# Kernel optimization log

Measured on AMD Instinct MI355X. Metric: run time of the kernel, lower is better.

Reference implementation:

```python
import jax, jax.numpy as jnp
import numpy as np

B, S, HID = 2, 1024, 2048
HQ, HKV, HD = 32, 8, 64
ROPE_BASE = 10000.0

def _rope_tables(seq_len, head_dim):
    inv_freq = 1.0 / (ROPE_BASE ** (np.arange(0, head_dim, 2, dtype=np.float32) / head_dim))
    t = np.arange(seq_len, dtype=np.float32)
    freqs = np.outer(t, inv_freq)                      # [S, d/2]
    emb = np.concatenate([freqs, freqs], axis=-1)      # [S, d]
    return jnp.asarray(np.cos(emb)), jnp.asarray(np.sin(emb))

def setup_inputs() -> dict:
    key = jax.random.key(0)
    ks = jax.random.split(key, 5)
    cos, sin = _rope_tables(S, HD)
    return {
        'hidden_states': jax.random.normal(ks[0], (B, S, HID), jnp.float32),
        'cos': cos, 'sin': sin,
        'Wq': jax.random.normal(ks[1], (HID, HID), jnp.float32) * (HID ** -0.5),
        'Wk': jax.random.normal(ks[2], (HID, HKV * HD), jnp.float32) * (HID ** -0.5),
        'Wv': jax.random.normal(ks[3], (HID, HKV * HD), jnp.float32) * (HID ** -0.5),
        'Wo': jax.random.normal(ks[4], (HID, HID), jnp.float32) * (HID ** -0.5),
    }

def _rotate_half(x):
    d = x.shape[-1]
    return jnp.concatenate([-x[..., d // 2:], x[..., :d // 2]], axis=-1)

def reference(hidden_states, cos, sin, Wq, Wk, Wv, Wo):
    b, s, _ = hidden_states.shape
    q = (hidden_states @ Wq).reshape(b, s, HQ, HD)    # [b,s,Hq,d]
    k = (hidden_states @ Wk).reshape(b, s, HKV, HD)   # [b,s,Hkv,d]
    v = (hidden_states @ Wv).reshape(b, s, HKV, HD)
    # RoPE: cos/sin [s,d] broadcast as [s,1,d] over head dim
    c = cos[:, None, :]
    sn = sin[:, None, :]
    q = q * c + _rotate_half(q) * sn
    k = k * c + _rotate_half(k) * sn
    # GQA: expand kv heads to query heads (repeat_kv)
    n_rep = HQ // HKV
    k = jnp.repeat(k, n_rep, axis=2)                  # [b,s,Hq,d]
    v = jnp.repeat(v, n_rep, axis=2)
    scale = HD ** -0.5
    scores = jnp.einsum('bqhd,bkhd->bhqk', q, k) * scale  # [b,Hq,s,s]
    causal = jnp.tril(jnp.ones((s, s), bool))
    scores = jnp.where(causal, scores, jnp.float32(-1e30))
    probs = jax.nn.softmax(scores.astype(jnp.float32), axis=-1).astype(q.dtype)
    out = jnp.einsum('bhqk,bkhd->bqhd', probs, v).reshape(b, s, HID)
    return out @ Wo
```

## Files before the change

kernel.cpp:

```cpp
#include <hip/hip_runtime.h>
#include <math.h>

#define B_   2
#define S_   1024
#define HID_ 2048
#define HQ_  32
#define HKV_ 8
#define HD_  64
#define NQKV 3072

#define PCHUNK 2097152

using short8  = __attribute__((ext_vector_type(8))) short;
using floatx4 = __attribute__((ext_vector_type(4))) float;

__device__ __forceinline__ unsigned short f2bf(float x) {
    unsigned int u = __builtin_bit_cast(unsigned int, x);
    u += 0x7FFFu + ((u >> 16) & 1u);
    return (unsigned short)(u >> 16);
}
__device__ __forceinline__ float bf2f(unsigned short u) {
    return __builtin_bit_cast(float, (unsigned int)u << 16);
}

__device__ __forceinline__ void gl_lds16(const unsigned short* g, unsigned short* l) {
    __builtin_amdgcn_global_load_lds(
        (const __attribute__((address_space(1))) void*)g,
        (__attribute__((address_space(3))) void*)l, 16, 0, 0);
}

__global__ __launch_bounds__(256) void gemm_qkv(const unsigned short* __restrict__ A,
                                                const unsigned short* __restrict__ Bt,
                                                unsigned short* __restrict__ Qp,
                                                unsigned short* __restrict__ KVp) {
    __shared__ __align__(16) unsigned short As[128 * 32];
    __shared__ __align__(16) unsigned short Bs[128 * 32];

    int bid = blockIdx.x;
    int m0, n0, z, Nw, nc0;
    unsigned short* C;
    if (bid < 512) {
        n0 = (bid & 15) * 128; m0 = ((bid >> 4) & 15) * 128; z = bid >> 8;
        C = Qp + (size_t)z * 2048 * 2048; Nw = 2048; nc0 = n0;
    } else {
        bid -= 512;
        n0 = 2048 + (bid & 7) * 128; m0 = ((bid >> 3) & 15) * 128; z = bid >> 7;
        C = KVp + (size_t)z * 2048 * 1024; Nw = 1024; nc0 = n0 - 2048;
    }
    const int kbase = z * 1024;

    const int tid  = threadIdx.x;
    const int w    = tid >> 6;
    const int lane = tid & 63;
    const int col  = lane & 15;
    const int quad = lane >> 4;
    const int wm = (w >> 1) * 64;
    const int wn = (w & 1) * 64;

    const int srow = lane >> 2;
    const int skof = (lane & 3) * 8;
    const unsigned short* Ag = A  + (size_t)(m0 + srow) * HID_ + skof;
    const unsigned short* Bg = Bt + (size_t)(n0 + srow) * HID_ + skof;
    const int rb = w * 16;

    floatx4 acc[4][4] = {};

    for (int k0 = kbase; k0 < kbase + 1024; k0 += 32) {
        gl_lds16(Ag + (size_t)(rb     ) * HID_ + k0, &As[(rb     ) * 32]);
        gl_lds16(Ag + (size_t)(rb + 64) * HID_ + k0, &As[(rb + 64) * 32]);
        gl_lds16(Bg + (size_t)(rb     ) * HID_ + k0, &Bs[(rb     ) * 32]);
        gl_lds16(Bg + (size_t)(rb + 64) * HID_ + k0, &Bs[(rb + 64) * 32]);
        __syncthreads();

        short8 af[4], bfr[4];
#pragma unroll
        for (int i = 0; i < 4; ++i)
            af[i] = *(const short8*)&As[(wm + i * 16 + col) * 32 + quad * 8];
#pragma unroll
        for (int j = 0; j < 4; ++j)
            bfr[j] = *(const short8*)&Bs[(wn + j * 16 + col) * 32 + quad * 8];
#pragma unroll
        for (int i = 0; i < 4; ++i)
#pragma unroll
            for (int j = 0; j < 4; ++j)
                acc[i][j] = __builtin_amdgcn_mfma_f32_16x16x32_bf16(
                    af[i], bfr[j], acc[i][j], 0, 0, 0);
        __syncthreads();
    }

#pragma unroll
    for (int i = 0; i < 4; ++i)
#pragma unroll
        for (int j = 0; j < 4; ++j)
#pragma unroll
            for (int r = 0; r < 4; ++r)
                C[(size_t)(m0 + wm + i * 16 + quad * 4 + r) * Nw
                  + (nc0 + wn + j * 16 + col)] = f2bf(acc[i][j][r]);
}

__global__ __launch_bounds__(256) void gemm_wo(const unsigned short* __restrict__ A,
                                               const unsigned short* __restrict__ Bt,
                                               float* __restrict__ Cf,
                                               unsigned short* __restrict__ Cp1) {
    __shared__ __align__(16) unsigned short As[128 * 32];
    __shared__ __align__(16) unsigned short Bs[128 * 32];

    const int m0 = blockIdx.y * 128;
    const int n0 = blockIdx.x * 128;
    const int z  = blockIdx.z;
    const int kbase = z * 1024;

    const int tid  = threadIdx.x;
    const int w    = tid >> 6;
    const int lane = tid & 63;
    const int col  = lane & 15;
    const int quad = lane >> 4;
    const int wm = (w >> 1) * 64;
    const int wn = (w & 1) * 64;

    const int srow = lane >> 2;
    const int skof = (lane & 3) * 8;
    const unsigned short* Ag = A  + (size_t)(m0 + srow) * HID_ + skof;
    const unsigned short* Bg = Bt + (size_t)(n0 + srow) * HID_ + skof;
    const int rb = w * 16;

    floatx4 acc[4][4] = {};

    for (int k0 = kbase; k0 < kbase + 1024; k0 += 32) {
        gl_lds16(Ag + (size_t)(rb     ) * HID_ + k0, &As[(rb     ) * 32]);
        gl_lds16(Ag + (size_t)(rb + 64) * HID_ + k0, &As[(rb + 64) * 32]);
        gl_lds16(Bg + (size_t)(rb     ) * HID_ + k0, &Bs[(rb     ) * 32]);
        gl_lds16(Bg + (size_t)(rb + 64) * HID_ + k0, &Bs[(rb + 64) * 32]);
        __syncthreads();

        short8 af[4], bfr[4];
#pragma unroll
        for (int i = 0; i < 4; ++i)
            af[i] = *(const short8*)&As[(wm + i * 16 + col) * 32 + quad * 8];
#pragma unroll
        for (int j = 0; j < 4; ++j)
            bfr[j] = *(const short8*)&Bs[(wn + j * 16 + col) * 32 + quad * 8];
#pragma unroll
        for (int i = 0; i < 4; ++i)
#pragma unroll
            for (int j = 0; j < 4; ++j)
                acc[i][j] = __builtin_amdgcn_mfma_f32_16x16x32_bf16(
                    af[i], bfr[j], acc[i][j], 0, 0, 0);
        __syncthreads();
    }

#pragma unroll
    for (int i = 0; i < 4; ++i)
#pragma unroll
        for (int j = 0; j < 4; ++j)
#pragma unroll
            for (int r = 0; r < 4; ++r) {
                size_t off = (size_t)(m0 + wm + i * 16 + quad * 4 + r) * HID_
                           + (n0 + wn + j * 16 + col);
                if (z == 0) Cf[off] = acc[i][j][r];
                else        Cp1[off] = f2bf(acc[i][j][r]);
            }
}

__global__ __launch_bounds__(256) void reduce_wo(float* __restrict__ out,
                                                 const unsigned short* __restrict__ p1) {
    int i4 = (blockIdx.x * 256 + threadIdx.x) * 4;
    float4 o = *(float4*)&out[i4];
    ushort4 p = *(const ushort4*)&p1[i4];
    o.x += bf2f(p.x); o.y += bf2f(p.y); o.z += bf2f(p.z); o.w += bf2f(p.w);
    *(float4*)&out[i4] = o;
}

__global__ __launch_bounds__(256) void convert_x(const float* __restrict__ in,
                                                 unsigned short* __restrict__ out) {
    int tid = blockIdx.x * 256 + threadIdx.x;
    float4 v = *(const float4*)&in[(size_t)tid * 4];
    ushort4 o = {f2bf(v.x), f2bf(v.y), f2bf(v.z), f2bf(v.w)};
    *(ushort4*)&out[(size_t)tid * 4] = o;
}

__global__ __launch_bounds__(256) void transpose_qkv(const float* __restrict__ Wq,
                                                     const float* __restrict__ Wk,
                                                     const float* __restrict__ Wv,
                                                     unsigned short* __restrict__ WcatT) {
    __shared__ float tile[32][33];
    int bid = blockIdx.x;
    const float* W;
    unsigned short* WT;
    int N, tn0, tk0;
    if (bid < 4096) {
        W = Wq; WT = WcatT; N = HID_;
        tn0 = (bid & 63) * 32; tk0 = (bid >> 6) * 32;
    } else if (bid < 5120) {
        bid -= 4096;
        W = Wk; WT = WcatT + (size_t)HID_ * HID_; N = 512;
        tn0 = (bid & 15) * 32; tk0 = (bid >> 4) * 32;
    } else {
        bid -= 5120;
        W = Wv; WT = WcatT + (size_t)(HID_ + 512) * HID_; N = 512;
        tn0 = (bid & 15) * 32; tk0 = (bid >> 4) * 32;
    }
    const int r  = threadIdx.x >> 3;
    const int c4 = (threadIdx.x & 7) * 4;
    float4 v = *(const float4*)&W[(size_t)(tk0 + r) * N + tn0 + c4];
    tile[r][c4 + 0] = v.x;
    tile[r][c4 + 1] = v.y;
    tile[r][c4 + 2] = v.z;
    tile[r][c4 + 3] = v.w;
    __syncthreads();
    ushort4 o = {f2bf(tile[c4 + 0][r]), f2bf(tile[c4 + 1][r]),
                 f2bf(tile[c4 + 2][r]), f2bf(tile[c4 + 3][r])};
    *(ushort4*)&WT[(size_t)(tn0 + r) * HID_ + tk0 + c4] = o;
}

__global__ __launch_bounds__(256) void transpose_wo(const float* __restrict__ Wo,
                                                    unsigned short* __restrict__ WoT) {
    __shared__ float tile[32][33];
    int bid = blockIdx.x;
    const int tn0 = (bid & 63) * 32;
    const int tk0 = (bid >> 6) * 32;
    const int r  = threadIdx.x >> 3;
    const int c4 = (threadIdx.x & 7) * 4;
    float4 v = *(const float4*)&Wo[(size_t)(tk0 + r) * HID_ + tn0 + c4];
    tile[r][c4 + 0] = v.x;
    tile[r][c4 + 1] = v.y;
    tile[r][c4 + 2] = v.z;
    tile[r][c4 + 3] = v.w;
    __syncthreads();
    ushort4 o = {f2bf(tile[c4 + 0][r]), f2bf(tile[c4 + 1][r]),
                 f2bf(tile[c4 + 2][r]), f2bf(tile[c4 + 3][r])};
    *(ushort4*)&WoT[(size_t)(tn0 + r) * HID_ + tk0 + c4] = o;
}

__global__ __launch_bounds__(256) void convert_qkv(const unsigned short* __restrict__ Qp,
                                                   const unsigned short* __restrict__ KVp,
                                                   const float* __restrict__ cosT,
                                                   const float* __restrict__ sinT,
                                                   unsigned short* __restrict__ Qbf,
                                                   unsigned short* __restrict__ Kbf,
                                                   unsigned short* __restrict__ Vt) {
    const size_t QSTR  = (size_t)2048 * 2048;
    const size_t KVSTR = (size_t)2048 * 1024;
    int tid = blockIdx.x * 256 + threadIdx.x;
    const int NQ = B_ * S_ * HQ_ * 32;
    const int NK = B_ * S_ * HKV_ * 32;
    if (tid < NQ) {
        int d = tid & 31;
        int h = (tid >> 5) & (HQ_ - 1);
        int s = (tid >> 10) & (S_ - 1);
        int b = tid >> 20;
        const unsigned short* row = Qp + (size_t)(b * S_ + s) * 2048 + h * HD_;
        float x0 = bf2f(row[d])      + bf2f(row[QSTR + d]);
        float x1 = bf2f(row[d + 32]) + bf2f(row[QSTR + d + 32]);
        float c0 = cosT[s * HD_ + d],      s0 = sinT[s * HD_ + d];
        float c1 = cosT[s * HD_ + d + 32], s1 = sinT[s * HD_ + d + 32];
        unsigned short* orow = Qbf + ((size_t)(b * HQ_ + h) * S_ + s) * HD_;
        orow[d]      = f2bf((x0 * c0 - x1 * s0) * 0.125f);
        orow[d + 32] = f2bf((x1 * c1 + x0 * s1) * 0.125f);
    } else if (tid < NQ + NK) {
        tid -= NQ;
        int d  = tid & 31;
        int kv = (tid >> 5) & (HKV_ - 1);
        int s  = (tid >> 8) & (S_ - 1);
        int b  = tid >> 18;
        const unsigned short* row = KVp + (size_t)(b * S_ + s) * 1024 + kv * HD_;
        float x0 = bf2f(row[d])      + bf2f(row[KVSTR + d]);
        float x1 = bf2f(row[d + 32]) + bf2f(row[KVSTR + d + 32]);
        float c0 = cosT[s * HD_ + d],      s0 = sinT[s * HD_ + d];
        float c1 = cosT[s * HD_ + d + 32], s1 = sinT[s * HD_ + d + 32];
        unsigned short* orow = Kbf + ((size_t)(b * HKV_ + kv) * S_ + s) * HD_;
        orow[d]      = f2bf(x0 * c0 - x1 * s0);
        orow[d + 32] = f2bf(x1 * c1 + x0 * s1);
    } else {
        tid -= NQ + NK;
        int s4 = tid & 255;
        int d  = (tid >> 8) & (HD_ - 1);
        int kv = (tid >> 14) & (HKV_ - 1);
        int b  = tid >> 17;
        int s  = s4 * 4;
        const unsigned short* base =
            KVp + ((size_t)(b * S_ + s)) * 1024 + 512 + kv * HD_ + d;
        ushort4 o;
#pragma unroll
        for (int j = 0; j < 4; ++j) {
            float v = bf2f(base[(size_t)j * 1024]) +
                      bf2f(base[KVSTR + (size_t)j * 1024]);
            ((unsigned short*)&o)[j] = f2bf(v);
        }
        *(ushort4*)&Vt[((size_t)(b * HKV_ + kv) * HD_ + d) * S_ + s] = o;
    }
}

__global__ __launch_bounds__(256) void attn_mfma(const unsigned short* __restrict__ Qbf,
                                                 const unsigned short* __restrict__ Kbf,
                                                 const unsigned short* __restrict__ Vt,
                                                 unsigned short* __restrict__ Ctx,
                                                 float* __restrict__ PO,
                                                 float* __restrict__ ML) {
    const int x  = blockIdx.x;
    const int kv = blockIdx.y;
    const int b  = blockIdx.z;

    int tq, chunk, it0, it1;
    if (x < 32) {
        tq = 16 + (x >> 1); chunk = x & 1;
        const int ns = (32 * tq + 95) >> 6;
        const int hh = ns >> 1;
        it0 = chunk ? hh : 0;
        it1 = chunk ? ns : hh;
    } else {
        tq = 47 - x; chunk = -1;
        it0 = 0;
        it1 = (32 * tq + 95) >> 6;
    }

    const int w    = threadIdx.x >> 6;
    const int lane = threadIdx.x & 63;
    const int col  = lane & 15;
    const int quad = lane >> 4;

    const int h   = kv * 4 + w;
    const int bh  = b * HQ_ + h;
    const int bkv = b * HKV_ + kv;
    const int qw  = 32 * tq;

    __shared__ __align__(16) unsigned short sK[2][64 * 64];
    __shared__ __align__(16) unsigned short sV[2][64 * 64];
    __shared__ __align__(16) unsigned short sP[4][16 * 64];
    unsigned short* myP = sP[w];

    short8 bq[2][2];
#pragma unroll
    for (int u = 0; u < 2; ++u) {
        const unsigned short* qrow = Qbf + ((size_t)bh * S_ + qw + 16 * u + col) * HD_;
        bq[u][0] = *(const short8*)&qrow[quad * 8];
        bq[u][1] = *(const short8*)&qrow[32 + quad * 8];
    }

    const unsigned short* Kbase = Kbf + (size_t)bkv * S_ * HD_;
    const unsigned short* Vbase = Vt  + (size_t)bkv * HD_ * S_;

    const int sr  = lane >> 3;
    const int ssl = (lane & 7) ^ sr;
    const int r0  = 16 * w;

    floatx4 acc[2][4] = {};
    float m_i[2] = {-1e30f, -1e30f};
    float l_i[2] = {0.f, 0.f};

    {
        const int kb = it0 * 64;
#pragma unroll
        for (int c = 0; c < 2; ++c) {
            const int row = r0 + 8 * c + sr;
            gl_lds16(Kbase + (size_t)(kb + row) * HD_ + ssl * 8, &sK[0][(r0 + 8 * c) * 64]);
            gl_lds16(Vbase + (size_t)row * S_ + kb + ssl * 8,    &sV[0][(r0 + 8 * c) * 64]);
        }
    }
    __syncthreads();

    int cur = 0;
    for (int it = it0; it < it1; ++it) {
        const int k0 = it * 64;

        if (it + 1 < it1) {
            const int kn = k0 + 64;
#pragma unroll
            for (int c = 0; c < 2; ++c) {
                const int row = r0 + 8 * c + sr;
                gl_lds16(Kbase + (size_t)(kn + row) * HD_ + ssl * 8,
                         &sK[cur ^ 1][(r0 + 8 * c) * 64]);
                gl_lds16(Vbase + (size_t)row * S_ + kn + ssl * 8,
                         &sV[cur ^ 1][(r0 + 8 * c) * 64]);
            }
        }

        floatx4 sc[2][4];
        __builtin_amdgcn_s_setprio(1);
#pragma unroll
        for (int tt = 0; tt < 4; ++tt) {
            const int krow = 16 * tt + col;
            const unsigned short* kr = &sK[cur][krow * 64];
            short8 ak0 = *(const short8*)&kr[((quad    ) ^ (krow & 7)) * 8];
            short8 ak1 = *(const short8*)&kr[((quad + 4) ^ (krow & 7)) * 8];
#pragma unroll
            for (int u = 0; u < 2; ++u) {
                floatx4 z = {0.f, 0.f, 0.f, 0.f};
                z = __builtin_amdgcn_mfma_f32_16x16x32_bf16(ak0, bq[u][0], z, 0, 0, 0);
                z = __builtin_amdgcn_mfma_f32_16x16x32_bf16(ak1, bq[u][1], z, 0, 0, 0);
                sc[u][tt] = z;
            }
        }
        __builtin_amdgcn_s_setprio(0);

        short8 pa[2][2];
#pragma unroll
        for (int u = 0; u < 2; ++u) {
            const int qbase = qw + 16 * u;
            const int myq   = qbase + col;
            if (k0 + 63 > qbase) {
#pragma unroll
                for (int tt = 0; tt < 4; ++tt)
#pragma unroll
                    for (int r = 0; r < 4; ++r)
                        if (k0 + 16 * tt + quad * 4 + r > myq) sc[u][tt][r] = -1e30f;
            }
            float vmax = sc[u][0][0];
#pragma unroll
            for (int tt = 0; tt < 4; ++tt)
#pragma unroll
                for (int r = 0; r < 4; ++r)
                    vmax = fmaxf(vmax, sc[u][tt][r]);
            vmax = fmaxf(vmax, __shfl_xor(vmax, 16, 64));
            vmax = fmaxf(vmax, __shfl_xor(vmax, 32, 64));

            if (!__all(vmax <= m_i[u] + 8.0f)) {
                const float mnew  = fmaxf(m_i[u], vmax);
                const float alpha = __expf(m_i[u] - mnew);
                m_i[u] = mnew;
                l_i[u] *= alpha;
#pragma unroll
                for (int nt = 0; nt < 4; ++nt)
#pragma unroll
                    for (int r = 0; r < 4; ++r)
                        acc[u][nt][r] *= alpha;
            }
            const float mu = m_i[u];

            float lsum = 0.f;
#pragma unroll
            for (int tt = 0; tt < 4; ++tt) {
                float p0 = __expf(sc[u][tt][0] - mu);
                float p1 = __expf(sc[u][tt][1] - mu);
                float p2 = __expf(sc[u][tt][2] - mu);
                float p3 = __expf(sc[u][tt][3] - mu);
                lsum += (p0 + p1) + (p2 + p3);
                ushort4 pk = {f2bf(p0), f2bf(p1), f2bf(p2), f2bf(p3)};
                *(ushort4*)&myP[col * 64
                                + ((((4 * tt + quad) >> 1) ^ (col & 7)) << 3)
                                + (quad & 1) * 4] = pk;
            }
            lsum += __shfl_xor(lsum, 16, 64);
            lsum += __shfl_xor(lsum, 32, 64);
            l_i[u] += lsum;

            pa[u][0] = *(const short8*)&myP[col * 64 + (((quad    ) ^ (col & 7)) << 3)];
            pa[u][1] = *(const short8*)&myP[col * 64 + (((4 + quad) ^ (col & 7)) << 3)];
        }

        __builtin_amdgcn_s_setprio(1);
#pragma unroll
        for (int nt = 0; nt < 4; ++nt) {
            const int vrow = 16 * nt + col;
            const unsigned short* vr = &sV[cur][vrow * 64];
            short8 vb0 = *(const short8*)&vr[((quad    ) ^ (vrow & 7)) * 8];
            short8 vb1 = *(const short8*)&vr[((quad + 4) ^ (vrow & 7)) * 8];
#pragma unroll
            for (int u = 0; u < 2; ++u) {
                acc[u][nt] = __builtin_amdgcn_mfma_f32_16x16x32_bf16(vb0, pa[u][0], acc[u][nt], 0, 0, 0);
                acc[u][nt] = __builtin_amdgcn_mfma_f32_16x16x32_bf16(vb1, pa[u][1], acc[u][nt], 0, 0, 0);
            }
        }
        __builtin_amdgcn_s_setprio(0);

        __syncthreads();
        cur ^= 1;
    }

    if (chunk < 0) {
#pragma unroll
        for (int u = 0; u < 2; ++u) {
            const float invl = 1.0f / l_i[u];
            unsigned short* crow =
                Ctx + (size_t)(b * S_ + qw + 16 * u + col) * HID_ + h * HD_;
#pragma unroll
            for (int nt = 0; nt < 4; ++nt) {
                ushort4 o = {f2bf(acc[u][nt][0] * invl), f2bf(acc[u][nt][1] * invl),
                             f2bf(acc[u][nt][2] * invl), f2bf(acc[u][nt][3] * invl)};
                *(ushort4*)&crow[nt * 16 + quad * 4] = o;
            }
        }
    } else {
        const int ts = tq - 16;
        const int base_row = (((b * 8 + kv) * 16 + ts) * 4 + w) * 32;
        float* POc = PO + (size_t)chunk * PCHUNK;
#pragma unroll
        for (int u = 0; u < 2; ++u) {
            float* prow = &POc[(size_t)(base_row + 16 * u + col) * 64];
#pragma unroll
            for (int nt = 0; nt < 4; ++nt)
                *(floatx4*)&prow[nt * 16 + quad * 4] = acc[u][nt];
            if (quad == 0) {
                const int rr = chunk * 32768 + base_row + 16 * u + col;
                ML[rr * 2 + 0] = m_i[u];
                ML[rr * 2 + 1] = l_i[u];
            }
        }
    }
}

__global__ __launch_bounds__(256) void merge_attn(const float* __restrict__ PO,
                                                  const float* __restrict__ ML,
                                                  unsigned short* __restrict__ Ctx) {
    const int tid = blockIdx.x * 256 + threadIdx.x;
    const int i4  = tid * 4;
    const int row = i4 >> 6;
    const int d0  = i4 & 63;

    const float m0 = ML[row * 2 + 0];
    const float l0 = ML[row * 2 + 1];
    const float m1 = ML[(32768 + row) * 2 + 0];
    const float l1 = ML[(32768 + row) * 2 + 1];
    const float mf = fmaxf(m0, m1);
    const float s0 = __expf(m0 - mf);
    const float s1 = __expf(m1 - mf);
    const float inv = 1.0f / (l0 * s0 + l1 * s1);

    float4 o0 = *(const float4*)&PO[(size_t)row * 64 + d0];
    float4 o1 = *(const float4*)&PO[(size_t)PCHUNK + (size_t)row * 64 + d0];

    const int q  = row & 31;
    const int hh = (row >> 5) & 3;
    const int ts = (row >> 7) & 15;
    const int kv = (row >> 11) & 7;
    const int b  = row >> 14;
    const int q_abs = 512 + ts * 32 + q;
    const int h_abs = kv * 4 + hh;

    ushort4 o;
    o.x = f2bf((o0.x * s0 + o1.x * s1) * inv);
    o.y = f2bf((o0.y * s0 + o1.y * s1) * inv);
    o.z = f2bf((o0.z * s0 + o1.z * s1) * inv);
    o.w = f2bf((o0.w * s0 + o1.w * s1) * inv);
    *(ushort4*)&Ctx[((size_t)(b * S_ + q_abs)) * HID_ + h_abs * HD_ + d0] = o;
}

extern "C" void kernel_launch(void* const* d_in, const int* in_sizes, int n_in,
                              void* d_out, int out_size, void* d_ws, size_t ws_size,
                              hipStream_t stream) {
    const float* X    = (const float*)d_in[0];
    const float* cosT = (const float*)d_in[1];
    const float* sinT = (const float*)d_in[2];
    const float* Wq   = (const float*)d_in[3];
    const float* Wk   = (const float*)d_in[4];
    const float* Wv   = (const float*)d_in[5];
    const float* Wo   = (const float*)d_in[6];

    const int M = B_ * S_;
    const size_t MB = 1024u * 1024u;

    char* ws = (char*)d_ws;
    unsigned short* Xbf   = (unsigned short*)(ws);
    unsigned short* Qbf   = (unsigned short*)(ws);
    unsigned short* WcatT = (unsigned short*)(ws + 8 * MB);
    unsigned short* Kbf   = (unsigned short*)(ws + 8 * MB);
    unsigned short* Vt    = (unsigned short*)(ws + 10 * MB);
    float*          MLb   = (float*)(ws + 12 * MB);
    unsigned short* WoT   = (unsigned short*)(ws + 12 * MB);
    unsigned short* KVp   = (unsigned short*)(ws + 20 * MB);
    unsigned short* Ctxbf = (unsigned short*)(ws + 20 * MB);
    unsigned short* Wop1  = (unsigned short*)(ws);
    unsigned short* Qp    = (unsigned short*)d_out;
    float*          PO    = (float*)d_out;
    float* out = (float*)d_out;

    convert_x<<<(M * HID_ / 4) / 256, 256, 0, stream>>>(X, Xbf);

    transpose_qkv<<<6144, 256, 0, stream>>>(Wq, Wk, Wv, WcatT);

    gemm_qkv<<<768, 256, 0, stream>>>(Xbf, WcatT, Qp, KVp);

    {
        int total = B_ * S_ * HQ_ * 32 + B_ * S_ * HKV_ * 32
                  + B_ * HKV_ * HD_ * (S_ / 4);
        convert_qkv<<<total / 256, 256, 0, stream>>>(Qp, KVp, cosT, sinT,
                                                     Qbf, Kbf, Vt);
    }

    attn_mfma<<<dim3(48, HKV_, B_), 256, 0, stream>>>(Qbf, Kbf, Vt, Ctxbf,
                                                      PO, MLb);

    merge_attn<<<2048, 256, 0, stream>>>(PO, MLb, Ctxbf);

    transpose_wo<<<4096, 256, 0, stream>>>(Wo, WoT);

    gemm_wo<<<dim3(16, 16, 2), 256, 0, stream>>>(Ctxbf, WoT, out, Wop1);

    reduce_wo<<<(M * HID_ / 4) / 256, 256, 0, stream>>>(out, Wop1);
}
```

Measured before the change: 246.6 us.

## Deepen GEMM K-tile with swizzled LDS, fuse prep kernels, vectorize RoPE conversion

```diff
diff --git a/kernel.cpp b/kernel.cpp
--- a/kernel.cpp
+++ b/kernel.cpp
@@ -33,8 +33,8 @@
                                                 const unsigned short* __restrict__ Bt,
                                                 unsigned short* __restrict__ Qp,
                                                 unsigned short* __restrict__ KVp) {
-    __shared__ __align__(16) unsigned short As[128 * 32];
-    __shared__ __align__(16) unsigned short Bs[128 * 32];
+    __shared__ __align__(16) unsigned short As[128 * 64];
+    __shared__ __align__(16) unsigned short Bs[128 * 64];
 
     int bid = blockIdx.x;
     int m0, n0, z, Nw, nc0;
@@ -57,34 +57,39 @@
     const int wm = (w >> 1) * 64;
     const int wn = (w & 1) * 64;
 
-    const int srow = lane >> 2;
-    const int skof = (lane & 3) * 8;
-    const unsigned short* Ag = A  + (size_t)(m0 + srow) * HID_ + skof;
-    const unsigned short* Bg = Bt + (size_t)(n0 + srow) * HID_ + skof;
-    const int rb = w * 16;
+    const int srow = lane >> 3;
+    const int scol = ((lane & 7) ^ srow) * 8;
+    const unsigned short* Ag = A  + (size_t)(m0 + w * 32 + srow) * HID_ + scol;
+    const unsigned short* Bg = Bt + (size_t)(n0 + w * 32 + srow) * HID_ + scol;
 
     floatx4 acc[4][4] = {};
 
-    for (int k0 = kbase; k0 < kbase + 1024; k0 += 32) {
-        gl_lds16(Ag + (size_t)(rb     ) * HID_ + k0, &As[(rb     ) * 32]);
-        gl_lds16(Ag + (size_t)(rb + 64) * HID_ + k0, &As[(rb + 64) * 32]);
-        gl_lds16(Bg + (size_t)(rb     ) * HID_ + k0, &Bs[(rb     ) * 32]);
-        gl_lds16(Bg + (size_t)(rb + 64) * HID_ + k0, &Bs[(rb + 64) * 32]);
+    for (int k0 = kbase; k0 < kbase + 1024; k0 += 64) {
+#pragma unroll
+        for (int c = 0; c < 4; ++c) {
+            gl_lds16(Ag + (size_t)(8 * c) * HID_ + k0, &As[(w * 32 + 8 * c) * 64]);
+            gl_lds16(Bg + (size_t)(8 * c) * HID_ + k0, &Bs[(w * 32 + 8 * c) * 64]);
+        }
         __syncthreads();
 
-        short8 af[4], bfr[4];
-#pragma unroll
-        for (int i = 0; i < 4; ++i)
-            af[i] = *(const short8*)&As[(wm + i * 16 + col) * 32 + quad * 8];
-#pragma unroll
-        for (int j = 0; j < 4; ++j)
-            bfr[j] = *(const short8*)&Bs[(wn + j * 16 + col) * 32 + quad * 8];
-#pragma unroll
-        for (int i = 0; i < 4; ++i)
+#pragma unroll
+        for (int hh = 0; hh < 2; ++hh) {
+            short8 af[4], bfr[4];
+#pragma unroll
+            for (int i = 0; i < 4; ++i)
+                af[i] = *(const short8*)&As[(wm + i * 16 + col) * 64
+                                            + (((hh * 4 + quad) ^ (col & 7)) << 3)];
 #pragma unroll
             for (int j = 0; j < 4; ++j)
-                acc[i][j] = __builtin_amdgcn_mfma_f32_16x16x32_bf16(
-                    af[i], bfr[j], acc[i][j], 0, 0, 0);
+                bfr[j] = *(const short8*)&Bs[(wn + j * 16 + col) * 64
+                                             + (((hh * 4 + quad) ^ (col & 7)) << 3)];
+#pragma unroll
+            for (int i = 0; i < 4; ++i)
+#pragma unroll
+                for (int j = 0; j < 4; ++j)
+                    acc[i][j] = __builtin_amdgcn_mfma_f32_16x16x32_bf16(
+                        af[i], bfr[j], acc[i][j], 0, 0, 0);
+        }
         __syncthreads();
     }
 
@@ -102,8 +107,8 @@
                                                const unsigned short* __restrict__ Bt,
                                                float* __restrict__ Cf,
                                                unsigned short* __restrict__ Cp1) {
-    __shared__ __align__(16) unsigned short As[128 * 32];
-    __shared__ __align__(16) unsigned short Bs[128 * 32];
+    __shared__ __align__(16) unsigned short As[128 * 64];
+    __shared__ __align__(16) unsigned short Bs[128 * 64];
 
     const int m0 = blockIdx.y * 128;
     const int n0 = blockIdx.x * 128;
@@ -118,34 +123,39 @@
     const int wm = (w >> 1) * 64;
     const int wn = (w & 1) * 64;
 
-    const int srow = lane >> 2;
-    const int skof = (lane & 3) * 8;
-    const unsigned short* Ag = A  + (size_t)(m0 + srow) * HID_ + skof;
-    const unsigned short* Bg = Bt + (size_t)(n0 + srow) * HID_ + skof;
-    const int rb = w * 16;
+    const int srow = lane >> 3;
+    const int scol = ((lane & 7) ^ srow) * 8;
+    const unsigned short* Ag = A  + (size_t)(m0 + w * 32 + srow) * HID_ + scol;
+    const unsigned short* Bg = Bt + (size_t)(n0 + w * 32 + srow) * HID_ + scol;
 
     floatx4 acc[4][4] = {};
 
-    for (int k0 = kbase; k0 < kbase + 1024; k0 += 32) {
-        gl_lds16(Ag + (size_t)(rb     ) * HID_ + k0, &As[(rb     ) * 32]);
-        gl_lds16(Ag + (size_t)(rb + 64) * HID_ + k0, &As[(rb + 64) * 32]);
-        gl_lds16(Bg + (size_t)(rb     ) * HID_ + k0, &Bs[(rb     ) * 32]);
-        gl_lds16(Bg + (size_t)(rb + 64) * HID_ + k0, &Bs[(rb + 64) * 32]);
+    for (int k0 = kbase; k0 < kbase + 1024; k0 += 64) {
+#pragma unroll
+        for (int c = 0; c < 4; ++c) {
+            gl_lds16(Ag + (size_t)(8 * c) * HID_ + k0, &As[(w * 32 + 8 * c) * 64]);
+            gl_lds16(Bg + (size_t)(8 * c) * HID_ + k0, &Bs[(w * 32 + 8 * c) * 64]);
+        }
         __syncthreads();
 
-        short8 af[4], bfr[4];
-#pragma unroll
-        for (int i = 0; i < 4; ++i)
-            af[i] = *(const short8*)&As[(wm + i * 16 + col) * 32 + quad * 8];
-#pragma unroll
-        for (int j = 0; j < 4; ++j)
-            bfr[j] = *(const short8*)&Bs[(wn + j * 16 + col) * 32 + quad * 8];
-#pragma unroll
-        for (int i = 0; i < 4; ++i)
+#pragma unroll
+        for (int hh = 0; hh < 2; ++hh) {
+            short8 af[4], bfr[4];
+#pragma unroll
+            for (int i = 0; i < 4; ++i)
+                af[i] = *(const short8*)&As[(wm + i * 16 + col) * 64
+                                            + (((hh * 4 + quad) ^ (col & 7)) << 3)];
 #pragma unroll
             for (int j = 0; j < 4; ++j)
-                acc[i][j] = __builtin_amdgcn_mfma_f32_16x16x32_bf16(
-                    af[i], bfr[j], acc[i][j], 0, 0, 0);
+                bfr[j] = *(const short8*)&Bs[(wn + j * 16 + col) * 64
+                                             + (((hh * 4 + quad) ^ (col & 7)) << 3)];
+#pragma unroll
+            for (int i = 0; i < 4; ++i)
+#pragma unroll
+                for (int j = 0; j < 4; ++j)
+                    acc[i][j] = __builtin_amdgcn_mfma_f32_16x16x32_bf16(
+                        af[i], bfr[j], acc[i][j], 0, 0, 0);
+        }
         __syncthreads();
     }
 
@@ -171,34 +181,44 @@
     *(float4*)&out[i4] = o;
 }
 
-__global__ __launch_bounds__(256) void convert_x(const float* __restrict__ in,
-                                                 unsigned short* __restrict__ out) {
-    int tid = blockIdx.x * 256 + threadIdx.x;
-    float4 v = *(const float4*)&in[(size_t)tid * 4];
-    ushort4 o = {f2bf(v.x), f2bf(v.y), f2bf(v.z), f2bf(v.w)};
-    *(ushort4*)&out[(size_t)tid * 4] = o;
-}
-
-__global__ __launch_bounds__(256) void transpose_qkv(const float* __restrict__ Wq,
-                                                     const float* __restrict__ Wk,
-                                                     const float* __restrict__ Wv,
-                                                     unsigned short* __restrict__ WcatT) {
+__global__ __launch_bounds__(256) void prep(const float* __restrict__ X,
+                                            const float* __restrict__ Wq,
+                                            const float* __restrict__ Wk,
+                                            const float* __restrict__ Wv,
+                                            const float* __restrict__ Wo,
+                                            unsigned short* __restrict__ Xbf,
+                                            unsigned short* __restrict__ WcatT,
+                                            unsigned short* __restrict__ WoT) {
     __shared__ float tile[32][33];
     int bid = blockIdx.x;
+    if (bid < 4096) {
+        int tid = bid * 256 + threadIdx.x;
+        float4 v = *(const float4*)&X[(size_t)tid * 4];
+        ushort4 o = {f2bf(v.x), f2bf(v.y), f2bf(v.z), f2bf(v.w)};
+        *(ushort4*)&Xbf[(size_t)tid * 4] = o;
+        return;
+    }
     const float* W;
     unsigned short* WT;
     int N, tn0, tk0;
-    if (bid < 4096) {
-        W = Wq; WT = WcatT; N = HID_;
+    if (bid < 10240) {
+        bid -= 4096;
+        if (bid < 4096) {
+            W = Wq; WT = WcatT; N = HID_;
+            tn0 = (bid & 63) * 32; tk0 = (bid >> 6) * 32;
+        } else if (bid < 5120) {
+            bid -= 4096;
+            W = Wk; WT = WcatT + (size_t)HID_ * HID_; N = 512;
+            tn0 = (bid & 15) * 32; tk0 = (bid >> 4) * 32;
+        } else {
+            bid -= 5120;
+            W = Wv; WT = WcatT + (size_t)(HID_ + 512) * HID_; N = 512;
+            tn0 = (bid & 15) * 32; tk0 = (bid >> 4) * 32;
+        }
+    } else {
+        bid -= 10240;
+        W = Wo; WT = WoT; N = HID_;
         tn0 = (bid & 63) * 32; tk0 = (bid >> 6) * 32;
-    } else if (bid < 5120) {
-        bid -= 4096;
-        W = Wk; WT = WcatT + (size_t)HID_ * HID_; N = 512;
-        tn0 = (bid & 15) * 32; tk0 = (bid >> 4) * 32;
-    } else {
-        bid -= 5120;
-        W = Wv; WT = WcatT + (size_t)(HID_ + 512) * HID_; N = 512;
-        tn0 = (bid & 15) * 32; tk0 = (bid >> 4) * 32;
     }
     const int r  = threadIdx.x >> 3;
     const int c4 = (threadIdx.x & 7) * 4;
@@ -242,37 +262,69 @@
     const size_t QSTR  = (size_t)2048 * 2048;
     const size_t KVSTR = (size_t)2048 * 1024;
     int tid = blockIdx.x * 256 + threadIdx.x;
-    const int NQ = B_ * S_ * HQ_ * 32;
-    const int NK = B_ * S_ * HKV_ * 32;
-    if (tid < NQ) {
-        int d = tid & 31;
-        int h = (tid >> 5) & (HQ_ - 1);
-        int s = (tid >> 10) & (S_ - 1);
-        int b = tid >> 20;
+    const int NQ4 = 524288;
+    const int NK4 = 131072;
+    if (tid < NQ4) {
+        int d0 = (tid & 7) * 4;
+        int h  = (tid >> 3) & 31;
+        int s  = (tid >> 8) & 1023;
+        int b  = tid >> 18;
         const unsigned short* row = Qp + (size_t)(b * S_ + s) * 2048 + h * HD_;
-        float x0 = bf2f(row[d])      + bf2f(row[QSTR + d]);
-        float x1 = bf2f(row[d + 32]) + bf2f(row[QSTR + d + 32]);
-        float c0 = cosT[s * HD_ + d],      s0 = sinT[s * HD_ + d];
-        float c1 = cosT[s * HD_ + d + 32], s1 = sinT[s * HD_ + d + 32];
+        ushort4 a0 = *(const ushort4*)&row[d0];
+        ushort4 a1 = *(const ushort4*)&row[d0 + 32];
+        ushort4 p0 = *(const ushort4*)&row[QSTR + d0];
+        ushort4 p1 = *(const ushort4*)&row[QSTR + d0 + 32];
+        float4 c0  = *(const float4*)&cosT[s * HD_ + d0];
+        float4 sn0 = *(const float4*)&sinT[s * HD_ + d0];
+        float4 c1  = *(const float4*)&cosT[s * HD_ + d0 + 32];
+        float4 sn1 = *(const float4*)&sinT[s * HD_ + d0 + 32];
+        ushort4 o0, o1;
+#pragma unroll
+        for (int j = 0; j < 4; ++j) {
+            float x0 = bf2f(((const unsigned short*)&a0)[j]) +
+                       bf2f(((const unsigned short*)&p0)[j]);
+            float x1 = bf2f(((const unsigned short*)&a1)[j]) +
+                       bf2f(((const unsigned short*)&p1)[j]);
+            ((unsigned short*)&o0)[j] =
+                f2bf((x0 * ((const float*)&c0)[j] - x1 * ((const float*)&sn0)[j]) * 0.125f);
+            ((unsigned short*)&o1)[j] =
+                f2bf((x1 * ((const float*)&c1)[j] + x0 * ((const float*)&sn1)[j]) * 0.125f);
+        }
         unsigned short* orow = Qbf + ((size_t)(b * HQ_ + h) * S_ + s) * HD_;
-        orow[d]      = f2bf((x0 * c0 - x1 * s0) * 0.125f);
-        orow[d + 32] = f2bf((x1 * c1 + x0 * s1) * 0.125f);
-    } else if (tid < NQ + NK) {
-        tid -= NQ;
-        int d  = tid & 31;
-        int kv = (tid >> 5) & (HKV_ - 1);
-        int s  = (tid >> 8) & (S_ - 1);
-        int b  = tid >> 18;
+        *(ushort4*)&orow[d0]      = o0;
+        *(ushort4*)&orow[d0 + 32] = o1;
+    } else if (tid < NQ4 + NK4) {
+        tid -= NQ4;
+        int d0 = (tid & 7) * 4;
+        int kv = (tid >> 3) & 7;
+        int s  = (tid >> 6) & 1023;
+        int b  = tid >> 16;
         const unsigned short* row = KVp + (size_t)(b * S_ + s) * 1024 + kv * HD_;
-        float x0 = bf2f(row[d])      + bf2f(row[KVSTR + d]);
-        float x1 = bf2f(row[d + 32]) + bf2f(row[KVSTR + d + 32]);
-        float c0 = cosT[s * HD_ + d],      s0 = sinT[s * HD_ + d];
-        float c1 = cosT[s * HD_ + d + 32], s1 = sinT[s * HD_ + d + 32];
+        ushort4 a0 = *(const ushort4*)&row[d0];
+        ushort4 a1 = *(const ushort4*)&row[d0 + 32];
+        ushort4 p0 = *(const ushort4*)&row[KVSTR + d0];
+        ushort4 p1 = *(const ushort4*)&row[KVSTR + d0 + 32];
+        float4 c0  = *(const float4*)&cosT[s * HD_ + d0];
+        float4 sn0 = *(const float4*)&sinT[s * HD_ + d0];
+        float4 c1  = *(const float4*)&cosT[s * HD_ + d0 + 32];
+        float4 sn1 = *(const float4*)&sinT[s * HD_ + d0 + 32];
+        ushort4 o0, o1;
+#pragma unroll
+        for (int j = 0; j < 4; ++j) {
+            float x0 = bf2f(((const unsigned short*)&a0)[j]) +
+                       bf2f(((const unsigned short*)&p0)[j]);
+            float x1 = bf2f(((const unsigned short*)&a1)[j]) +
+                       bf2f(((const unsigned short*)&p1)[j]);
+            ((unsigned short*)&o0)[j] =
+                f2bf(x0 * ((const float*)&c0)[j] - x1 * ((const float*)&sn0)[j]);
+            ((unsigned short*)&o1)[j] =
+                f2bf(x1 * ((const float*)&c1)[j] + x0 * ((const float*)&sn1)[j]);
+        }
         unsigned short* orow = Kbf + ((size_t)(b * HKV_ + kv) * S_ + s) * HD_;
-        orow[d]      = f2bf(x0 * c0 - x1 * s0);
-        orow[d + 32] = f2bf(x1 * c1 + x0 * s1);
+        *(ushort4*)&orow[d0]      = o0;
+        *(ushort4*)&orow[d0 + 32] = o1;
     } else {
-        tid -= NQ + NK;
+        tid -= NQ4 + NK4;
         int s4 = tid & 255;
         int d  = (tid >> 8) & (HD_ - 1);
         int kv = (tid >> 14) & (HKV_ - 1);
@@ -550,13 +602,15 @@
     const size_t MB = 1024u * 1024u;
 
     char* ws = (char*)d_ws;
+    const bool bigws = ws_size >= 40 * MB;
+
     unsigned short* Xbf   = (unsigned short*)(ws);
     unsigned short* Qbf   = (unsigned short*)(ws);
     unsigned short* WcatT = (unsigned short*)(ws + 8 * MB);
     unsigned short* Kbf   = (unsigned short*)(ws + 8 * MB);
     unsigned short* Vt    = (unsigned short*)(ws + 10 * MB);
-    float*          MLb   = (float*)(ws + 12 * MB);
-    unsigned short* WoT   = (unsigned short*)(ws + 12 * MB);
+    unsigned short* WoT   = (unsigned short*)(ws + (bigws ? 28 : 12) * MB);
+    float*          MLb   = (float*)(ws + (bigws ? 36 : 12) * MB);
     unsigned short* KVp   = (unsigned short*)(ws + 20 * MB);
     unsigned short* Ctxbf = (unsigned short*)(ws + 20 * MB);
     unsigned short* Wop1  = (unsigned short*)(ws);
@@ -564,25 +618,20 @@
     float*          PO    = (float*)d_out;
     float* out = (float*)d_out;
 
-    convert_x<<<(M * HID_ / 4) / 256, 256, 0, stream>>>(X, Xbf);
-
-    transpose_qkv<<<6144, 256, 0, stream>>>(Wq, Wk, Wv, WcatT);
+    prep<<<bigws ? 14336 : 10240, 256, 0, stream>>>(X, Wq, Wk, Wv, Wo,
+                                                    Xbf, WcatT, WoT);
 
     gemm_qkv<<<768, 256, 0, stream>>>(Xbf, WcatT, Qp, KVp);
 
-    {
-        int total = B_ * S_ * HQ_ * 32 + B_ * S_ * HKV_ * 32
-                  + B_ * HKV_ * HD_ * (S_ / 4);
-        convert_qkv<<<total / 256, 256, 0, stream>>>(Qp, KVp, cosT, sinT,
-                                                     Qbf, Kbf, Vt);
-    }
+    convert_qkv<<<3584, 256, 0, stream>>>(Qp, KVp, cosT, sinT, Qbf, Kbf, Vt);
 
     attn_mfma<<<dim3(48, HKV_, B_), 256, 0, stream>>>(Qbf, Kbf, Vt, Ctxbf,
                                                       PO, MLb);
 
     merge_attn<<<2048, 256, 0, stream>>>(PO, MLb, Ctxbf);
 
-    transpose_wo<<<4096, 256, 0, stream>>>(Wo, WoT);
+    if (!bigws)
+        transpose_wo<<<4096, 256, 0, stream>>>(Wo, WoT);
 
     gemm_wo<<<dim3(16, 16, 2), 256, 0, stream>>>(Ctxbf, WoT, out, Wop1);
 
```

Result: faster. 229.2 us (-7.1%).
